# Performance work log

Hardware: AMD Instinct MI355X
Metric: run time of the kernel (lower is better)

The kernel has to match this reference:

```python
import jax, jax.numpy as jnp
import numpy as np

B, N, D, R, NUM_HEADS, S = 8, 512, 256, 6, 3, 1000


def setup_inputs() -> dict:
    key = jax.random.key(0)
    ks = jax.random.split(key, 12)
    init = lambda k, shape: jax.random.normal(k, shape, jnp.float32) * 0.02
    return {
        "symbol_ids": jax.random.randint(ks[0], (B, N), 0, S),
        "positions": jax.random.normal(ks[1], (B, N, 2), jnp.float32),
        "sym_table": init(ks[2], (S, D)),
        "layer_table": init(ks[3], (S, D)),      # layer-0 interpretation embedding
        "rel_W": init(ks[4], (R, D, D)),          # per-relation Linear weights (in,out)
        "rel_b": init(ks[5], (R, D)),
        "h1_W": init(ks[6], (NUM_HEADS, D, D)),   # interpretation head Linear1
        "h1_b": init(ks[7], (NUM_HEADS, D)),
        "h2_W": init(ks[8], (NUM_HEADS, D)),      # interpretation head Linear2 (D->1)
        "h2_b": init(ks[9], (NUM_HEADS,)),
        "out_W": init(ks[10], (D, D)),
        "out_b": init(ks[11], (D,)),
    }


def _relation_type(dx, dy):
    # Vectorized version of PositionalGrammar._get_relation_type (if/elif chain)
    return jnp.select(
        [dy > 0.5, dy < -0.5, dx < -0.5, dx > 0.5,
         (jnp.abs(dx) < 0.3) & (jnp.abs(dy) < 0.3)],
        [0, 1, 2, 3, 4], 5)


def _positional_grammar(symbols, positions, rel_W, rel_b):
    # transformed[b,j] = symbols[b,j] + sum_{i!=j} (symbols[b,i] @ W_r(i,j) + b_r(i,j))
    dx = positions[:, None, :, 0] - positions[:, :, None, 0]  # [b,i,j]
    dy = positions[:, None, :, 1] - positions[:, :, None, 1]
    rel = _relation_type(dx, dy)                               # [b,i,j] int
    n = symbols.shape[1]
    not_self = ~jnp.eye(n, dtype=bool)
    # one-hot relation mask, self-pairs excluded: [b,i,j,r]
    M = ((rel[..., None] == jnp.arange(R)) & not_self[None, :, :, None]).astype(symbols.dtype)
    T = jnp.einsum('bid,rde->brie', symbols, rel_W)            # per-relation transform of sources
    contrib = jnp.einsum('bijr,brie->bje', M, T)               # scatter-add over sources i
    bias = jnp.einsum('bijr,re->bje', M, rel_b)                # per-pair bias accumulation
    return symbols + contrib + bias


def reference(symbol_ids, positions, sym_table, layer_table, rel_W, rel_b,
              h1_W, h1_b, h2_W, h2_b, out_W, out_b):
    # SymbolEmbedding (calendar_pos=None path; layer=0)
    symbols = sym_table[symbol_ids] + layer_table[symbol_ids]  # [B,N,D]
    # PositionalGrammar
    symbols = _positional_grammar(symbols, positions, rel_W, rel_b)
    # LayeredInterpretation: 3 heads of Linear-GELU-Linear(D->1)
    h = jax.nn.gelu(jnp.einsum('bnd,rde->brne', symbols, h1_W)
                    + h1_b[None, :, None, :], approximate=False)
    interp = jnp.einsum('brne,re->brn', h, h2_W) + h2_b[None, :, None]  # [B,3,N]
    # output projection
    output = symbols @ out_W + out_b
    return (output,
            interp[:, 0, :, None],   # exoteric  [B,N,1]
            interp[:, 1, :, None],   # esoteric
            interp[:, 2, :, None],   # sacred
            symbols)
```

## Files before the change

kernel.cpp:

```cpp
#include <hip/hip_runtime.h>
#include <hip/hip_bf16.h>
#include <math.h>

#define BB 8
#define NN 512
#define DD 256
#define BNT 4096

typedef __attribute__((ext_vector_type(8))) short short8;
typedef __attribute__((ext_vector_type(4))) float f32x4;

#define OFF_S0B   0u
#define OFF_TT    524288u
#define OFF_WCT   6815744u
#define OFF_WBT   7012352u
#define OFF_BB    7143424u
#define OFF_REL   7144448u

#define OUT0_OFF   0u
#define INTERP_OFF 1048576u
#define SYM_OFF    1060864u

__device__ __forceinline__ float gelu_exact(float x) {
    return 0.5f * x * (1.0f + erff(x * 0.70710678118654752f));
}

__device__ __forceinline__ ushort f2bf(float x) {
    __hip_bfloat16 h = __float2bfloat16(x);
    union { __hip_bfloat16 b; ushort u; } cv;
    cv.b = h;
    return cv.u;
}

__device__ __forceinline__ int rel_of(float dx, float dy) {
    int r = (fabsf(dx) < 0.3f && fabsf(dy) < 0.3f) ? 4 : 5;
    r = (dx >  0.5f) ? 3 : r;
    r = (dx < -0.5f) ? 2 : r;
    r = (dy < -0.5f) ? 1 : r;
    r = (dy >  0.5f) ? 0 : r;
    return r;
}

#define TILE_IDS()                                             \
    const int lane = tid & 63, w = tid >> 6;                   \
    const int wm = w >> 1, wn = w & 1;                         \
    const int quad = lane >> 4, l15 = lane & 15;               \
    const int sm = tid >> 2, sq = tid & 3;

#define MFMA_STEP()                                                          \
    {                                                                        \
        short8 af[2], bfr[2];                                                \
        _Pragma("unroll")                                                    \
        for (int mt = 0; mt < 2; mt++)                                       \
            af[mt] = *(const short8*)&Als[(quad * 64 + wm * 32 + mt * 16 + l15) * 8]; \
        _Pragma("unroll")                                                    \
        for (int nt = 0; nt < 2; nt++)                                       \
            bfr[nt] = *(const short8*)&Bls[(quad * 64 + wn * 32 + nt * 16 + l15) * 8]; \
        _Pragma("unroll")                                                    \
        for (int mt = 0; mt < 2; mt++)                                       \
            _Pragma("unroll")                                                \
            for (int nt = 0; nt < 2; nt++)                                   \
                acc[mt][nt] = __builtin_amdgcn_mfma_f32_16x16x32_bf16(       \
                    af[mt], bfr[nt], acc[mt][nt], 0, 0, 0);                  \
    }

#define ACC_INIT()                                             \
    f32x4 acc[2][2];                                           \
    _Pragma("unroll") for (int mt = 0; mt < 2; mt++)           \
    _Pragma("unroll") for (int nt = 0; nt < 2; nt++)           \
        acc[mt][nt] = (f32x4){0.f, 0.f, 0.f, 0.f};

__global__ __launch_bounds__(256) void prep_kernel(
    const float* __restrict__ relW, const float* __restrict__ h1W,
    const float* __restrict__ outW, const float* __restrict__ h1b,
    const float* __restrict__ outb, const float* __restrict__ h2b,
    ushort* __restrict__ WcT, ushort* __restrict__ WbT,
    float* __restrict__ bbig, float* __restrict__ outI)
{
    int idx = blockIdx.x * 256 + threadIdx.x;
    {
        int e = idx / 1536, k = idx - e * 1536;
        int r = k >> 8, d = k & 255;
        WcT[idx] = f2bf(relW[(r * DD + d) * DD + e]);
    }
    if (idx < 262144) {
        int c = idx >> 8, d = idx & 255;
        float v;
        if (c < 768) { int r = c >> 8, e = c & 255; v = h1W[(r * DD + d) * DD + e]; }
        else         { v = outW[d * DD + (c - 768)]; }
        WbT[idx] = f2bf(v);
    }
    if (idx < 3 * BNT) outI[idx] = h2b[idx >> 12];
    if (idx < 1024) bbig[idx] = (idx < 768) ? h1b[idx] : outb[idx - 768];
}

__global__ __launch_bounds__(256) void gather_kernel(
    const int* __restrict__ ids, const float* __restrict__ symt,
    const float* __restrict__ layt, float* __restrict__ symOut,
    ushort* __restrict__ s0b)
{
    int row = blockIdx.x, c = threadIdx.x;
    int id = ids[row];
    float v = symt[id * DD + c] + layt[id * DD + c];
    symOut[(size_t)row * DD + c] = v;
    s0b[(size_t)row * DD + c] = f2bf(v);
}

__global__ __launch_bounds__(256) void classify_kernel(
    const float* __restrict__ positions, unsigned char* __restrict__ rel)
{
    int b = blockIdx.x >> 6;
    int j0 = (blockIdx.x & 63) << 3;
    int tid = threadIdx.x;
    int jl = tid >> 5, sub = tid & 31;
    __shared__ float px[NN], py[NN];
    for (int i = tid; i < NN; i += 256) {
        float2 p = ((const float2*)positions)[b * NN + i];
        px[i] = p.x; py[i] = p.y;
    }
    __syncthreads();
    int j = j0 + jl;
    float xj = px[j], yj = py[j];
    union { unsigned char u8[16]; uint4 v; } codes;
#pragma unroll
    for (int t = 0; t < 16; t++) {
        int i = sub * 16 + t;
        int r = rel_of(xj - px[i], yj - py[i]);
        r = (i == j) ? 6 : r;
        codes.u8[t] = (unsigned char)r;
    }
    *(uint4*)&rel[((size_t)(b * NN + j)) * NN + sub * 16] = codes.v;
}

__global__ __launch_bounds__(256) void gemmT_kernel(
    const ushort* __restrict__ WcT, const ushort* __restrict__ s0b,
    const float* __restrict__ relb, ushort* __restrict__ TT)
{
    __shared__ ushort Als[2048], Bls[2048];
    int tid = threadIdx.x;
    int b = blockIdx.z;
    int rowM0 = blockIdx.y * 64;
    int col0 = blockIdx.x * 64;
    int r = rowM0 >> 8, e0 = rowM0 & 255;
    TILE_IDS();
    ACC_INIT();
    const ushort* gA = WcT + (size_t)(e0 + sm) * 1536 + r * 256 + sq * 8;
    const ushort* gB = s0b + ((size_t)(b * NN) + col0 + sm) * DD + sq * 8;

    for (int k0 = 0; k0 < DD; k0 += 32) {
        uint4 av = *(const uint4*)(gA + k0);
        uint4 bv = *(const uint4*)(gB + k0);
        __syncthreads();
        *(uint4*)&Als[(sq * 64 + sm) * 8] = av;
        *(uint4*)&Bls[(sq * 64 + sm) * 8] = bv;
        __syncthreads();
        MFMA_STEP();
    }
#pragma unroll
    for (int mt = 0; mt < 2; mt++)
#pragma unroll
        for (int nt = 0; nt < 2; nt++)
#pragma unroll
            for (int v = 0; v < 4; v++) {
                int e = e0 + wm * 32 + mt * 16 + quad * 4 + v;
                int i = col0 + wn * 32 + nt * 16 + l15;
                TT[((size_t)(b * DD) + e) * 3072 + r * 512 + i] =
                    f2bf(acc[mt][nt][v] + relb[r * DD + e]);
            }
}

__global__ __launch_bounds__(256) void agg_gemm(
    const unsigned char* __restrict__ rel, const ushort* __restrict__ TT,
    float* __restrict__ symOut)
{
    __shared__ ushort Als[2048], Bls[2048];
    int tid = threadIdx.x;
    int z = blockIdx.z, b = z >> 2, rg = z & 3;
    b = z / 3; rg = z - b * 3;
    int row0 = blockIdx.y * 64, col0 = blockIdx.x * 64;
    TILE_IDS();
    ACC_INIT();
    const unsigned char* gC = rel + ((size_t)(b * NN + row0 + sm)) * NN;
    const ushort* gB = TT + ((size_t)(b * DD) + col0 + sm) * 3072 + rg * 1024 + sq * 8;

    for (int k0 = 0; k0 < 1024; k0 += 32) {
        int kk = k0 + sq * 8;
        int r = 2 * rg + (k0 >> 9);
        int i0 = (rg * 1024 + kk) & 511;
        uint2 cw = *(const uint2*)(gC + i0);
        uint4 bv = *(const uint4*)(gB + k0);
        union alignas(16) { ushort u[8]; uint4 v; } am;
#pragma unroll
        for (int t = 0; t < 8; t++) {
            unsigned int word = (t < 4) ? cw.x : cw.y;
            unsigned int code = (word >> (8 * (t & 3))) & 255u;
            am.u[t] = (code == (unsigned)r) ? 0x3F80 : 0;
        }
        __syncthreads();
        *(uint4*)&Als[(sq * 64 + sm) * 8] = am.v;
        *(uint4*)&Bls[(sq * 64 + sm) * 8] = bv;
        __syncthreads();
        MFMA_STEP();
    }
#pragma unroll
    for (int mt = 0; mt < 2; mt++)
#pragma unroll
        for (int nt = 0; nt < 2; nt++)
#pragma unroll
            for (int v = 0; v < 4; v++) {
                int j = row0 + wm * 32 + mt * 16 + quad * 4 + v;
                int e = col0 + wn * 32 + nt * 16 + l15;
                atomicAdd(&symOut[((size_t)(b * NN) + j) * DD + e], acc[mt][nt][v]);
            }
}

__global__ __launch_bounds__(256) void gemm2_kernel(
    const float* __restrict__ symOut, const ushort* __restrict__ WbT,
    const float* __restrict__ bbig, const float* __restrict__ h2W,
    float* __restrict__ out0, float* __restrict__ outI)
{
    __shared__ ushort Als[2048], Bls[2048];
    int tid = threadIdx.x;
    int row0 = blockIdx.y * 64, col0 = blockIdx.x * 64;
    TILE_IDS();
    ACC_INIT();
    const float*  gA = symOut + (size_t)(row0 + sm) * DD + sq * 8;
    const ushort* gB = WbT    + (size_t)(col0 + sm) * DD + sq * 8;

    for (int k0 = 0; k0 < DD; k0 += 32) {
        union alignas(16) { float f[8]; float4 v4[2]; } af32;
        af32.v4[0] = *(const float4*)(gA + k0);
        af32.v4[1] = *(const float4*)(gA + k0 + 4);
        uint4 bv = *(const uint4*)(gB + k0);
        union alignas(16) { ushort u[8]; uint4 v; } am;
#pragma unroll
        for (int t = 0; t < 8; t++) am.u[t] = f2bf(af32.f[t]);
        __syncthreads();
        *(uint4*)&Als[(sq * 64 + sm) * 8] = am.v;
        *(uint4*)&Bls[(sq * 64 + sm) * 8] = bv;
        __syncthreads();
        MFMA_STEP();
    }
    if (col0 >= 768) {
#pragma unroll
        for (int nt = 0; nt < 2; nt++) {
            int c = col0 + wn * 32 + nt * 16 + l15;
            float bb = bbig[c];
#pragma unroll
            for (int mt = 0; mt < 2; mt++)
#pragma unroll
                for (int v = 0; v < 4; v++) {
                    int row = row0 + wm * 32 + mt * 16 + quad * 4 + v;
                    out0[(size_t)row * DD + (c - 768)] = acc[mt][nt][v] + bb;
                }
        }
    } else {
        int head = col0 >> 8;
        float part[2][4];
#pragma unroll
        for (int mt = 0; mt < 2; mt++)
#pragma unroll
            for (int v = 0; v < 4; v++) part[mt][v] = 0.f;
#pragma unroll
        for (int nt = 0; nt < 2; nt++) {
            int c = col0 + wn * 32 + nt * 16 + l15;
            float bb = bbig[c];
            float w2 = h2W[c];
#pragma unroll
            for (int mt = 0; mt < 2; mt++)
#pragma unroll
                for (int v = 0; v < 4; v++)
                    part[mt][v] += gelu_exact(acc[mt][nt][v] + bb) * w2;
        }
#pragma unroll
        for (int mt = 0; mt < 2; mt++)
#pragma unroll
            for (int v = 0; v < 4; v++) {
                float p = part[mt][v];
                p += __shfl_xor(p, 1); p += __shfl_xor(p, 2);
                p += __shfl_xor(p, 4); p += __shfl_xor(p, 8);
                if (l15 == 0) {
                    int row = row0 + wm * 32 + mt * 16 + quad * 4 + v;
                    atomicAdd(&outI[head * BNT + row], p);
                }
            }
    }
}

extern "C" void kernel_launch(void* const* d_in, const int* in_sizes, int n_in,
                              void* d_out, int out_size, void* d_ws, size_t ws_size,
                              hipStream_t stream)
{
    const int*   ids  = (const int*)d_in[0];
    const float* pos  = (const float*)d_in[1];
    const float* symt = (const float*)d_in[2];
    const float* layt = (const float*)d_in[3];
    const float* relW = (const float*)d_in[4];
    const float* relb = (const float*)d_in[5];
    const float* h1W  = (const float*)d_in[6];
    const float* h1b  = (const float*)d_in[7];
    const float* h2W  = (const float*)d_in[8];
    const float* h2b  = (const float*)d_in[9];
    const float* outW = (const float*)d_in[10];
    const float* outb = (const float*)d_in[11];
    float* out = (float*)d_out;
    float* ws  = (float*)d_ws;

    ushort* s0b  = (ushort*)(ws + OFF_S0B);
    ushort* TT   = (ushort*)(ws + OFF_TT);
    ushort* WcT  = (ushort*)(ws + OFF_WCT);
    ushort* WbT  = (ushort*)(ws + OFF_WBT);
    float*  bbig = ws + OFF_BB;
    unsigned char* rel = (unsigned char*)(ws + OFF_REL);

    prep_kernel<<<1536, 256, 0, stream>>>(relW, h1W, outW, h1b, outb, h2b,
                                          WcT, WbT, bbig, out + INTERP_OFF);
    gather_kernel<<<4096, 256, 0, stream>>>(ids, symt, layt, out + SYM_OFF, s0b);
    classify_kernel<<<512, 256, 0, stream>>>(pos, rel);
    gemmT_kernel<<<dim3(8, 24, 8), 256, 0, stream>>>(WcT, s0b, relb, TT);
    agg_gemm<<<dim3(4, 8, 24), 256, 0, stream>>>(rel, TT, out + SYM_OFF);
    gemm2_kernel<<<dim3(16, 64), 256, 0, stream>>>(out + SYM_OFF, WbT,
                                                   bbig, h2W,
                                                   out + OUT0_OFF, out + INTERP_OFF);
}
```

Before: 143.7 us.

## Double-buffer LDS tiles in GEMM kernels and merge front-end kernels into one launch

The three GEMM kernels now use two LDS buffers, so the next K-slice's global loads are issued before the current MFMA step and staged afterwards. This removes one barrier per iteration and hides load latency behind compute. Separately, the prep, gather and classify kernels are merged into a single front kernel that dispatches on block index, saving two launches. The cost is doubled shared memory per block, which may lower occupancy, plus more live registers for the prefetched data.

```diff
diff --git a/kernel.cpp b/kernel.cpp
--- a/kernel.cpp
+++ b/kernel.cpp
@@ -47,15 +47,15 @@
     const int quad = lane >> 4, l15 = lane & 15;               \
     const int sm = tid >> 2, sq = tid & 3;
 
-#define MFMA_STEP()                                                          \
+#define MFMA_STEP(Abuf, Bbuf)                                                \
     {                                                                        \
         short8 af[2], bfr[2];                                                \
         _Pragma("unroll")                                                    \
         for (int mt = 0; mt < 2; mt++)                                       \
-            af[mt] = *(const short8*)&Als[(quad * 64 + wm * 32 + mt * 16 + l15) * 8]; \
+            af[mt] = *(const short8*)&(Abuf)[(quad * 64 + wm * 32 + mt * 16 + l15) * 8]; \
         _Pragma("unroll")                                                    \
         for (int nt = 0; nt < 2; nt++)                                       \
-            bfr[nt] = *(const short8*)&Bls[(quad * 64 + wn * 32 + nt * 16 + l15) * 8]; \
+            bfr[nt] = *(const short8*)&(Bbuf)[(quad * 64 + wn * 32 + nt * 16 + l15) * 8]; \
         _Pragma("unroll")                                                    \
         for (int mt = 0; mt < 2; mt++)                                       \
             _Pragma("unroll")                                                \
@@ -70,73 +70,70 @@
     _Pragma("unroll") for (int nt = 0; nt < 2; nt++)           \
         acc[mt][nt] = (f32x4){0.f, 0.f, 0.f, 0.f};
 
-__global__ __launch_bounds__(256) void prep_kernel(
+__global__ __launch_bounds__(256) void front_kernel(
+    const int* __restrict__ ids, const float* __restrict__ positions,
+    const float* __restrict__ symt, const float* __restrict__ layt,
     const float* __restrict__ relW, const float* __restrict__ h1W,
     const float* __restrict__ outW, const float* __restrict__ h1b,
     const float* __restrict__ outb, const float* __restrict__ h2b,
     ushort* __restrict__ WcT, ushort* __restrict__ WbT,
-    float* __restrict__ bbig, float* __restrict__ outI)
-{
-    int idx = blockIdx.x * 256 + threadIdx.x;
-    {
-        int e = idx / 1536, k = idx - e * 1536;
-        int r = k >> 8, d = k & 255;
-        WcT[idx] = f2bf(relW[(r * DD + d) * DD + e]);
-    }
-    if (idx < 262144) {
-        int c = idx >> 8, d = idx & 255;
-        float v;
-        if (c < 768) { int r = c >> 8, e = c & 255; v = h1W[(r * DD + d) * DD + e]; }
-        else         { v = outW[d * DD + (c - 768)]; }
-        WbT[idx] = f2bf(v);
-    }
-    if (idx < 3 * BNT) outI[idx] = h2b[idx >> 12];
-    if (idx < 1024) bbig[idx] = (idx < 768) ? h1b[idx] : outb[idx - 768];
-}
-
-__global__ __launch_bounds__(256) void gather_kernel(
-    const int* __restrict__ ids, const float* __restrict__ symt,
-    const float* __restrict__ layt, float* __restrict__ symOut,
-    ushort* __restrict__ s0b)
-{
-    int row = blockIdx.x, c = threadIdx.x;
-    int id = ids[row];
-    float v = symt[id * DD + c] + layt[id * DD + c];
-    symOut[(size_t)row * DD + c] = v;
-    s0b[(size_t)row * DD + c] = f2bf(v);
-}
-
-__global__ __launch_bounds__(256) void classify_kernel(
-    const float* __restrict__ positions, unsigned char* __restrict__ rel)
-{
-    int b = blockIdx.x >> 6;
-    int j0 = (blockIdx.x & 63) << 3;
-    int tid = threadIdx.x;
-    int jl = tid >> 5, sub = tid & 31;
+    float* __restrict__ bbig, float* __restrict__ outI,
+    float* __restrict__ symOut, ushort* __restrict__ s0b,
+    unsigned char* __restrict__ rel)
+{
     __shared__ float px[NN], py[NN];
-    for (int i = tid; i < NN; i += 256) {
-        float2 p = ((const float2*)positions)[b * NN + i];
-        px[i] = p.x; py[i] = p.y;
-    }
-    __syncthreads();
-    int j = j0 + jl;
-    float xj = px[j], yj = py[j];
-    union { unsigned char u8[16]; uint4 v; } codes;
-#pragma unroll
-    for (int t = 0; t < 16; t++) {
-        int i = sub * 16 + t;
-        int r = rel_of(xj - px[i], yj - py[i]);
-        r = (i == j) ? 6 : r;
-        codes.u8[t] = (unsigned char)r;
-    }
-    *(uint4*)&rel[((size_t)(b * NN + j)) * NN + sub * 16] = codes.v;
+    int blk = blockIdx.x, tid = threadIdx.x;
+    if (blk < 1536) {
+        int idx = blk * 256 + tid;
+        {
+            int e = idx / 1536, k = idx - e * 1536;
+            int r = k >> 8, d = k & 255;
+            WcT[idx] = f2bf(relW[(r * DD + d) * DD + e]);
+        }
+        if (idx < 262144) {
+            int c = idx >> 8, d = idx & 255;
+            float v;
+            if (c < 768) { int r = c >> 8, e = c & 255; v = h1W[(r * DD + d) * DD + e]; }
+            else         { v = outW[d * DD + (c - 768)]; }
+            WbT[idx] = f2bf(v);
+        }
+        if (idx < 3 * BNT) outI[idx] = h2b[idx >> 12];
+        if (idx < 1024) bbig[idx] = (idx < 768) ? h1b[idx] : outb[idx - 768];
+    } else if (blk < 5632) {
+        int row = blk - 1536;
+        int id = ids[row];
+        float v = symt[id * DD + tid] + layt[id * DD + tid];
+        symOut[(size_t)row * DD + tid] = v;
+        s0b[(size_t)row * DD + tid] = f2bf(v);
+    } else {
+        int blk2 = blk - 5632;
+        int b = blk2 >> 6;
+        int j0 = (blk2 & 63) << 3;
+        int jl = tid >> 5, sub = tid & 31;
+        for (int i = tid; i < NN; i += 256) {
+            float2 p = ((const float2*)positions)[b * NN + i];
+            px[i] = p.x; py[i] = p.y;
+        }
+        __syncthreads();
+        int j = j0 + jl;
+        float xj = px[j], yj = py[j];
+        union { unsigned char u8[16]; uint4 v; } codes;
+#pragma unroll
+        for (int t = 0; t < 16; t++) {
+            int i = sub * 16 + t;
+            int r = rel_of(xj - px[i], yj - py[i]);
+            r = (i == j) ? 6 : r;
+            codes.u8[t] = (unsigned char)r;
+        }
+        *(uint4*)&rel[((size_t)(b * NN + j)) * NN + sub * 16] = codes.v;
+    }
 }
 
 __global__ __launch_bounds__(256) void gemmT_kernel(
     const ushort* __restrict__ WcT, const ushort* __restrict__ s0b,
     const float* __restrict__ relb, ushort* __restrict__ TT)
 {
-    __shared__ ushort Als[2048], Bls[2048];
+    __shared__ ushort Als[2][2048], Bls[2][2048];
     int tid = threadIdx.x;
     int b = blockIdx.z;
     int rowM0 = blockIdx.y * 64;
@@ -146,15 +143,23 @@
     ACC_INIT();
     const ushort* gA = WcT + (size_t)(e0 + sm) * 1536 + r * 256 + sq * 8;
     const ushort* gB = s0b + ((size_t)(b * NN) + col0 + sm) * DD + sq * 8;
-
-    for (int k0 = 0; k0 < DD; k0 += 32) {
-        uint4 av = *(const uint4*)(gA + k0);
-        uint4 bv = *(const uint4*)(gB + k0);
+    const int lo = (sq * 64 + sm) * 8;
+
+    *(uint4*)&Als[0][lo] = *(const uint4*)gA;
+    *(uint4*)&Bls[0][lo] = *(const uint4*)gB;
+#pragma unroll
+    for (int i = 0; i < 8; i++) {
         __syncthreads();
-        *(uint4*)&Als[(sq * 64 + sm) * 8] = av;
-        *(uint4*)&Bls[(sq * 64 + sm) * 8] = bv;
-        __syncthreads();
-        MFMA_STEP();
+        uint4 av2, bv2;
+        if (i < 7) {
+            av2 = *(const uint4*)(gA + (i + 1) * 32);
+            bv2 = *(const uint4*)(gB + (i + 1) * 32);
+        }
+        MFMA_STEP(Als[i & 1], Bls[i & 1]);
+        if (i < 7) {
+            *(uint4*)&Als[(i + 1) & 1][lo] = av2;
+            *(uint4*)&Bls[(i + 1) & 1][lo] = bv2;
+        }
     }
 #pragma unroll
     for (int mt = 0; mt < 2; mt++)
@@ -173,35 +178,47 @@
     const unsigned char* __restrict__ rel, const ushort* __restrict__ TT,
     float* __restrict__ symOut)
 {
-    __shared__ ushort Als[2048], Bls[2048];
+    __shared__ ushort Als[2][2048], Bls[2][2048];
     int tid = threadIdx.x;
-    int z = blockIdx.z, b = z >> 2, rg = z & 3;
-    b = z / 3; rg = z - b * 3;
+    int z = blockIdx.z;
+    int b = z / 3, rg = z - b * 3;
     int row0 = blockIdx.y * 64, col0 = blockIdx.x * 64;
     TILE_IDS();
     ACC_INIT();
     const unsigned char* gC = rel + ((size_t)(b * NN + row0 + sm)) * NN;
     const ushort* gB = TT + ((size_t)(b * DD) + col0 + sm) * 3072 + rg * 1024 + sq * 8;
-
-    for (int k0 = 0; k0 < 1024; k0 += 32) {
-        int kk = k0 + sq * 8;
-        int r = 2 * rg + (k0 >> 9);
-        int i0 = (rg * 1024 + kk) & 511;
-        uint2 cw = *(const uint2*)(gC + i0);
-        uint4 bv = *(const uint4*)(gB + k0);
-        union alignas(16) { ushort u[8]; uint4 v; } am;
-#pragma unroll
-        for (int t = 0; t < 8; t++) {
-            unsigned int word = (t < 4) ? cw.x : cw.y;
-            unsigned int code = (word >> (8 * (t & 3))) & 255u;
-            am.u[t] = (code == (unsigned)r) ? 0x3F80 : 0;
-        }
+    const int lo = (sq * 64 + sm) * 8;
+
+#define AGG_LOADS(i, cw, bv)                                        \
+    cw = *(const uint2*)(gC + (((i) * 32 + sq * 8) & 511));         \
+    bv = *(const uint4*)(gB + (i) * 32);
+
+#define AGG_STAGE(i, cw, bv, buf)                                   \
+    {                                                               \
+        int rr_ = 2 * rg + (((i) * 32) >> 9);                       \
+        union alignas(16) { ushort u[8]; uint4 v; } am;             \
+        _Pragma("unroll")                                           \
+        for (int t = 0; t < 8; t++) {                               \
+            unsigned int word = (t < 4) ? cw.x : cw.y;              \
+            unsigned int code = (word >> (8 * (t & 3))) & 255u;     \
+            am.u[t] = (code == (unsigned)rr_) ? 0x3F80 : 0;         \
+        }                                                           \
+        *(uint4*)&Als[buf][lo] = am.v;                              \
+        *(uint4*)&Bls[buf][lo] = bv;                                \
+    }
+
+    uint2 cw0; uint4 bv0;
+    AGG_LOADS(0, cw0, bv0);
+    AGG_STAGE(0, cw0, bv0, 0);
+    for (int i = 0; i < 32; i++) {
         __syncthreads();
-        *(uint4*)&Als[(sq * 64 + sm) * 8] = am.v;
-        *(uint4*)&Bls[(sq * 64 + sm) * 8] = bv;
-        __syncthreads();
-        MFMA_STEP();
-    }
+        uint2 cw2; uint4 bv2;
+        if (i < 31) { AGG_LOADS(i + 1, cw2, bv2); }
+        MFMA_STEP(Als[i & 1], Bls[i & 1]);
+        if (i < 31) { AGG_STAGE(i + 1, cw2, bv2, (i + 1) & 1); }
+    }
+#undef AGG_LOADS
+#undef AGG_STAGE
 #pragma unroll
     for (int mt = 0; mt < 2; mt++)
 #pragma unroll
@@ -219,28 +236,44 @@
     const float* __restrict__ bbig, const float* __restrict__ h2W,
     float* __restrict__ out0, float* __restrict__ outI)
 {
-    __shared__ ushort Als[2048], Bls[2048];
+    __shared__ ushort Als[2][2048], Bls[2][2048];
     int tid = threadIdx.x;
     int row0 = blockIdx.y * 64, col0 = blockIdx.x * 64;
     TILE_IDS();
     ACC_INIT();
     const float*  gA = symOut + (size_t)(row0 + sm) * DD + sq * 8;
     const ushort* gB = WbT    + (size_t)(col0 + sm) * DD + sq * 8;
-
-    for (int k0 = 0; k0 < DD; k0 += 32) {
-        union alignas(16) { float f[8]; float4 v4[2]; } af32;
-        af32.v4[0] = *(const float4*)(gA + k0);
-        af32.v4[1] = *(const float4*)(gA + k0 + 4);
-        uint4 bv = *(const uint4*)(gB + k0);
-        union alignas(16) { ushort u[8]; uint4 v; } am;
-#pragma unroll
-        for (int t = 0; t < 8; t++) am.u[t] = f2bf(af32.f[t]);
+    const int lo = (sq * 64 + sm) * 8;
+
+#define G2_LOADS(i, a0, a1, bv)                                     \
+    a0 = *(const float4*)(gA + (i) * 32);                           \
+    a1 = *(const float4*)(gA + (i) * 32 + 4);                       \
+    bv = *(const uint4*)(gB + (i) * 32);
+
+#define G2_STAGE(a0, a1, bv, buf)                                   \
+    {                                                               \
+        union alignas(16) { ushort u[8]; uint4 v; } am;             \
+        am.u[0] = f2bf(a0.x); am.u[1] = f2bf(a0.y);                 \
+        am.u[2] = f2bf(a0.z); am.u[3] = f2bf(a0.w);                 \
+        am.u[4] = f2bf(a1.x); am.u[5] = f2bf(a1.y);                 \
+        am.u[6] = f2bf(a1.z); am.u[7] = f2bf(a1.w);                 \
+        *(uint4*)&Als[buf][lo] = am.v;                              \
+        *(uint4*)&Bls[buf][lo] = bv;                                \
+    }
+
+    float4 a0, a1; uint4 bv;
+    G2_LOADS(0, a0, a1, bv);
+    G2_STAGE(a0, a1, bv, 0);
+#pragma unroll
+    for (int i = 0; i < 8; i++) {
         __syncthreads();
-        *(uint4*)&Als[(sq * 64 + sm) * 8] = am.v;
-        *(uint4*)&Bls[(sq * 64 + sm) * 8] = bv;
-        __syncthreads();
-        MFMA_STEP();
-    }
+        float4 a0n, a1n; uint4 bvn;
+        if (i < 7) { G2_LOADS(i + 1, a0n, a1n, bvn); }
+        MFMA_STEP(Als[i & 1], Bls[i & 1]);
+        if (i < 7) { G2_STAGE(a0n, a1n, bvn, (i + 1) & 1); }
+    }
+#undef G2_LOADS
+#undef G2_STAGE
     if (col0 >= 768) {
 #pragma unroll
         for (int nt = 0; nt < 2; nt++) {
@@ -313,10 +346,9 @@
     float*  bbig = ws + OFF_BB;
     unsigned char* rel = (unsigned char*)(ws + OFF_REL);
 
-    prep_kernel<<<1536, 256, 0, stream>>>(relW, h1W, outW, h1b, outb, h2b,
-                                          WcT, WbT, bbig, out + INTERP_OFF);
-    gather_kernel<<<4096, 256, 0, stream>>>(ids, symt, layt, out + SYM_OFF, s0b);
-    classify_kernel<<<512, 256, 0, stream>>>(pos, rel);
+    front_kernel<<<6144, 256, 0, stream>>>(ids, pos, symt, layt, relW, h1W, outW,
+                                           h1b, outb, h2b, WcT, WbT, bbig,
+                                           out + INTERP_OFF, out + SYM_OFF, s0b, rel);
     gemmT_kernel<<<dim3(8, 24, 8), 256, 0, stream>>>(WcT, s0b, relb, TT);
     agg_gemm<<<dim3(4, 8, 24), 256, 0, stream>>>(rel, TT, out + SYM_OFF);
     gemm2_kernel<<<dim3(16, 64), 256, 0, stream>>>(out + SYM_OFF, WbT,
```

Measured after the change: 139.8 us. 2.7% less time.
